# Optimization experiments

Measured on AMD Instinct MI355X. Metric: run time of the kernel, lower is better.

Reference implementation:

```python
import jax, jax.numpy as jnp
import numpy as np
from jax import lax

B, N, C, T = 8, 2000, 32, 12
K, F_CHEV, F_TIME = 3, 64, 64
LN_EPS = 1e-5


def setup_inputs() -> dict:
    key = jax.random.key(0)
    ks = jax.random.split(key, 20)
    s = 0.1
    return {
        "x": jax.random.normal(ks[0], (B, N, C, T), jnp.float32),
        "cheb_polys": jax.random.normal(ks[1], (K, N, N), jnp.float32) * 0.02,
        # temporal attention params
        "U1": jax.random.normal(ks[2], (N,), jnp.float32) * s,
        "U2": jax.random.normal(ks[3], (C, N), jnp.float32) * s,
        "U3": jax.random.normal(ks[4], (C,), jnp.float32) * s,
        "be": jax.random.normal(ks[5], (1, T, T), jnp.float32) * s,
        "Ve": jax.random.normal(ks[6], (T, T), jnp.float32) * s,
        # spatial attention params
        "W1": jax.random.normal(ks[7], (T,), jnp.float32) * s,
        "W2": jax.random.normal(ks[8], (C, T), jnp.float32) * s,
        "W3": jax.random.normal(ks[9], (C,), jnp.float32) * s,
        "bs": jax.random.normal(ks[10], (1, N, N), jnp.float32) * s,
        "Vs": jax.random.normal(ks[11], (N, N), jnp.float32) * (s / np.sqrt(N)),
        # Chebyshev conv params, stacked (K, C, F_chev)
        "Theta": jax.random.normal(ks[12], (K, C, F_CHEV), jnp.float32) * (1.0 / np.sqrt(C)),
        # time conv (1x3) and residual conv (1x1), NCHW/OIHW layout
        "tc_w": jax.random.normal(ks[13], (F_TIME, F_CHEV, 1, 3), jnp.float32) * (1.0 / np.sqrt(3 * F_CHEV)),
        "tc_b": jnp.zeros((F_TIME,), jnp.float32),
        "rc_w": jax.random.normal(ks[14], (F_TIME, C, 1, 1), jnp.float32) * (1.0 / np.sqrt(C)),
        "rc_b": jnp.zeros((F_TIME,), jnp.float32),
        # LayerNorm over nb_time_filter
        "ln_g": jnp.ones((F_TIME,), jnp.float32),
        "ln_b": jnp.zeros((F_TIME,), jnp.float32),
    }


def _conv2d(x, w, b, stride_t):
    # x: (B, Cin, N, T), w: (Cout, Cin, kh, kw)
    pad_w = (w.shape[3] - 1) // 2
    y = lax.conv_general_dilated(
        x, w, window_strides=(1, stride_t),
        padding=[(0, 0), (pad_w, pad_w)],
        dimension_numbers=("NCHW", "OIHW", "NCHW"))
    return y + b[None, :, None, None]


def reference(x, cheb_polys, U1, U2, U3, be, Ve, W1, W2, W3, bs, Vs,
              Theta, tc_w, tc_b, rc_w, rc_b, ln_g, ln_b):
    b, n, c, t = x.shape

    # ---- temporal attention: (B, T, T) ----
    lhs = jnp.einsum("bnct,n->btc", x, U1)              # x.permute(0,3,2,1) @ U1
    lhs = jnp.einsum("btc,cn->btn", lhs, U2)
    rhs = jnp.einsum("c,bnct->bnt", U3, x)
    E = jnp.einsum("ij,bjk->bik", Ve,
                   jax.nn.sigmoid(jnp.einsum("btn,bnu->btu", lhs, rhs) + be))
    temporal_At = jax.nn.softmax(E, axis=1)             # (B, T, T)

    # apply temporal attention
    x_TAt = jnp.matmul(x.reshape(b, n * c, t), temporal_At).reshape(b, n, c, t)

    # ---- spatial attention on x_TAt: (B, N, N) ----
    lhs_s = jnp.einsum("bnct,t->bnc", x_TAt, W1)
    lhs_s = jnp.einsum("bnc,ct->bnt", lhs_s, W2)
    rhs_s = jnp.einsum("c,bnct->btn", W3, x_TAt)        # (W3 @ x).transpose(-1,-2)
    S = jnp.einsum("ij,bjk->bik", Vs,
                   jax.nn.sigmoid(jnp.einsum("bnt,btm->bnm", lhs_s, rhs_s) + bs))
    spatial_At = jax.nn.softmax(S, axis=1)              # (B, N, N)

    # ---- Chebyshev graph conv with spatial attention ----
    # A[b,k,j,i] = cheb[k,j,i] * SAt[b,j,i]; out = relu(sum_k A^T x Theta_k)
    A = cheb_polys[None, :, :, :] * spatial_At[:, None, :, :]   # (B, K, N, N)
    h = jnp.einsum("bkji,bjct->bkitc", A, x)                    # (B, K, N, T, C)
    spatial_gcn = jax.nn.relu(jnp.einsum("bkitc,kcf->bift", h, Theta))  # (B, N, F, T)

    # ---- temporal conv + residual + LayerNorm ----
    time_out = _conv2d(spatial_gcn.transpose(0, 2, 1, 3), tc_w, tc_b, 1)  # (B, F_time, N, T')
    x_res = _conv2d(x.transpose(0, 2, 1, 3), rc_w, rc_b, 1)               # (B, F_time, N, T')
    z = jax.nn.relu(x_res + time_out).transpose(0, 3, 2, 1)               # (B, T', N, F_time)

    mu = jnp.mean(z, axis=-1, keepdims=True)
    var = jnp.mean((z - mu) ** 2, axis=-1, keepdims=True)
    zn = (z - mu) * lax.rsqrt(var + LN_EPS) * ln_g + ln_b

    return zn.transpose(0, 2, 3, 1)                                       # (B, N, F_time, T')
```

## Files before the change

### kernel.cpp

```cpp
#include <hip/hip_runtime.h>
#include <hip/hip_bf16.h>
#include <math.h>

#define B_ 8
#define N_ 2000
#define C_ 32
#define T_ 12
#define K_ 3
#define FC_ 64
#define FT_ 64
#define PW 2048

typedef short bf16x8 __attribute__((ext_vector_type(8)));
typedef float f32x4 __attribute__((ext_vector_type(4)));

__device__ __forceinline__ float sigmoidf(float v) { return 1.0f / (1.0f + __expf(-v)); }
__device__ __forceinline__ float bf2f(unsigned short u) {
    union { unsigned int i; float f; } v; v.i = ((unsigned int)u) << 16; return v.f;
}
__device__ __forceinline__ unsigned short f2bf(float f) {
    union { __hip_bfloat16 h; unsigned short u; } v; v.h = __float2bfloat16(f); return v.u;
}
typedef const __attribute__((address_space(1))) void* gas_t;
typedef __attribute__((address_space(3))) void* las_t;
__device__ __forceinline__ void gload16(const unsigned short* g, unsigned short* l) {
    __builtin_amdgcn_global_load_lds((gas_t)g, (las_t)l, 16, 0, 0);
}

__global__ __launch_bounds__(256) void k_tprep(const float* __restrict__ x, const float* __restrict__ U1,
                                               const float* __restrict__ U3,
                                               float* __restrict__ rhsT, float* __restrict__ plh) {
    int b = blockIdx.y, chunk = blockIdx.x;
    int tid = threadIdx.x;
    int nl = tid >> 5, c = tid & 31;
    int w = tid >> 6;
    float u3 = U3[c];
    float plA[12];
#pragma unroll
    for (int t = 0; t < 12; ++t) plA[t] = 0.f;
    for (int it = 0; it < 5; ++it) {
        int n = chunk * 40 + it * 8 + nl;
        const float* xp = x + ((size_t)(b * 2000 + n) * 32 + c) * 12;
        float4 v0 = *(const float4*)xp, v1 = *(const float4*)(xp + 4), v2 = *(const float4*)(xp + 8);
        float xv[12] = {v0.x, v0.y, v0.z, v0.w, v1.x, v1.y, v1.z, v1.w, v2.x, v2.y, v2.z, v2.w};
        float rv[12];
#pragma unroll
        for (int t = 0; t < 12; ++t) rv[t] = u3 * xv[t];
#pragma unroll
        for (int off = 16; off >= 1; off >>= 1)
#pragma unroll
            for (int t = 0; t < 12; ++t) rv[t] += __shfl_xor(rv[t], off);
        if (c == 0) {
#pragma unroll
            for (int t = 0; t < 12; ++t) rhsT[(size_t)(b * 2000 + n) * 12 + t] = rv[t];
        }
        float u1 = U1[n];
#pragma unroll
        for (int t = 0; t < 12; ++t) plA[t] += u1 * xv[t];
    }
#pragma unroll
    for (int t = 0; t < 12; ++t) plA[t] += __shfl_xor(plA[t], 32);
    __shared__ float accs[4][32][12];
    if ((tid & 63) < 32) {
#pragma unroll
        for (int t = 0; t < 12; ++t) accs[w][c][t] = plA[t];
    }
    __syncthreads();
    if (tid < 384) {
        int c2 = tid / 12, t2 = tid % 12;
        float s = accs[0][c2][t2] + accs[1][c2][t2] + accs[2][c2][t2] + accs[3][c2][t2];
        plh[((size_t)(b * 50 + chunk)) * 384 + tid] = s;
    }
}

__global__ __launch_bounds__(256) void k_tred(const float* __restrict__ plh, float* __restrict__ lhs1) {
    int b = blockIdx.x;
    for (int q = threadIdx.x; q < 384; q += 256) {
        const float* p = plh + (size_t)b * 50 * 384 + q;
        float s = 0.f;
        for (int ch = 0; ch < 50; ++ch) s += p[(size_t)ch * 384];
        int c = q / 12, t = q % 12;
        lhs1[(b * 12 + t) * 32 + c] = s;
    }
}

__global__ __launch_bounds__(256) void k_lhsT(const float* __restrict__ lhs1, const float* __restrict__ U2,
                                              float* __restrict__ lhsT) {
    int gid = blockIdx.x * 256 + threadIdx.x;
    if (gid >= B_ * T_ * N_) return;
    int n = gid % N_;
    int bt = gid / N_;
    const float* l1 = lhs1 + bt * C_;
    float a = 0.f;
#pragma unroll
    for (int c = 0; c < C_; ++c) a += l1[c] * U2[c * N_ + n];
    lhsT[gid] = a;
}

__global__ __launch_bounds__(256) void k_tatt1(const float* __restrict__ lhsT, const float* __restrict__ rhsT,
                                               float* __restrict__ pP) {
    int b = blockIdx.y, ch = blockIdx.x;
    int tid = threadIdx.x;
    int n0 = ch * 125;
    __shared__ float sL[12][128];
    __shared__ float sR[128][12];
    for (int q = tid; q < 12 * 125; q += 256) {
        int t = q / 125, nn = q % 125;
        sL[t][nn] = lhsT[(size_t)(b * 12 + t) * 2000 + n0 + nn];
    }
    for (int q = tid; q < 125 * 12; q += 256) {
        int nn = q / 12, t = q % 12;
        sR[nn][t] = rhsT[(size_t)(b * 2000 + n0 + nn) * 12 + t];
    }
    __syncthreads();
    if (tid < 144) {
        int tP = tid / 12, uP = tid % 12;
        float a = 0.f;
#pragma unroll 5
        for (int nn = 0; nn < 125; ++nn) a += sL[tP][nn] * sR[nn][uP];
        pP[(size_t)(b * 16 + ch) * 144 + tid] = a;
    }
}

__global__ __launch_bounds__(256) void k_tatt2(const float* __restrict__ pP, const float* __restrict__ be,
                                               const float* __restrict__ Ve, float* __restrict__ At) {
    int b = blockIdx.x, tid = threadIdx.x;
    __shared__ float sp[144], sE[144], mk[12], sk[12];
    int tP = tid / 12, uP = tid % 12;
    if (tid < 144) {
        float a = 0.f;
#pragma unroll
        for (int ch = 0; ch < 16; ++ch) a += pP[(size_t)(b * 16 + ch) * 144 + tid];
        sp[tid] = sigmoidf(a + be[tid]);
    }
    __syncthreads();
    if (tid < 144) {
        float e = 0.f;
#pragma unroll
        for (int j = 0; j < 12; ++j) e += Ve[tP * 12 + j] * sp[j * 12 + uP];
        sE[tid] = e;
    }
    __syncthreads();
    if (tid < 12) {
        float m = -1e30f;
#pragma unroll
        for (int i = 0; i < 12; ++i) m = fmaxf(m, sE[i * 12 + tid]);
        float s = 0.f;
#pragma unroll
        for (int i = 0; i < 12; ++i) s += __expf(sE[i * 12 + tid] - m);
        mk[tid] = m; sk[tid] = 1.0f / s;
    }
    __syncthreads();
    if (tid < 144) At[b * 144 + tid] = __expf(sE[tid] - mk[uP]) * sk[uP];
}

__global__ __launch_bounds__(256) void k_xsp(const float* __restrict__ x, const float* __restrict__ At,
                                             const float* __restrict__ W1, const float* __restrict__ W2,
                                             const float* __restrict__ W3,
                                             float* __restrict__ lhs_s, float* __restrict__ rhs_s) {
    int b = blockIdx.y, chunk = blockIdx.x;
    int tid = threadIdx.x, nl = tid >> 5, c = tid & 31;
    int n = chunk * 8 + nl;
    __shared__ float atl[144];
    __shared__ float w2l[384];
    __shared__ float w1l[12];
    if (tid < 144) atl[tid] = At[b * 144 + tid];
    if (tid >= 144 && tid < 156) w1l[tid - 144] = W1[tid - 144];
    for (int q = tid; q < 384; q += 256) w2l[q] = W2[q];
    __syncthreads();
    const float* xp = x + ((size_t)(b * 2000 + n) * 32 + c) * 12;
    float4 v0 = *(const float4*)xp, v1 = *(const float4*)(xp + 4), v2 = *(const float4*)(xp + 8);
    float xv[12] = {v0.x, v0.y, v0.z, v0.w, v1.x, v1.y, v1.z, v1.w, v2.x, v2.y, v2.z, v2.w};
    float xa[12];
#pragma unroll
    for (int t = 0; t < 12; ++t) {
        float s = 0.f;
#pragma unroll
        for (int u = 0; u < 12; ++u) s += xv[u] * atl[u * 12 + t];
        xa[t] = s;
    }
    float w3 = W3[c];
    float rv[12], lv[12];
    float l1 = 0.f;
#pragma unroll
    for (int t = 0; t < 12; ++t) l1 += xa[t] * w1l[t];
#pragma unroll
    for (int t = 0; t < 12; ++t) { rv[t] = w3 * xa[t]; lv[t] = l1 * w2l[c * 12 + t]; }
#pragma unroll
    for (int off = 16; off >= 1; off >>= 1)
#pragma unroll
        for (int t = 0; t < 12; ++t) { rv[t] += __shfl_xor(rv[t], off); lv[t] += __shfl_xor(lv[t], off); }
    if (c == 0) {
#pragma unroll
        for (int t = 0; t < 12; ++t) rhs_s[(size_t)(b * 12 + t) * 2000 + n] = rv[t];
#pragma unroll
        for (int t = 0; t < 12; ++t) lhs_s[(size_t)(b * 2000 + n) * 12 + t] = lv[t];
    }
}

__global__ __launch_bounds__(256) void k_wprep(const float* __restrict__ tc_w, const float* __restrict__ rc_w,
                                               float* __restrict__ tcwT, float* __restrict__ rcwT) {
    int gid = blockIdx.x * 256 + threadIdx.x;
    if (gid < 12288) {
        int fi = gid / 192, rem = gid % 192, f = rem / 3, d = rem % 3;
        tcwT[gid] = tc_w[(f * 64 + fi) * 3 + d];
    } else if (gid < 14336) {
        int q = gid - 12288;
        int c = q >> 6, f = q & 63;
        rcwT[q] = rc_w[f * 32 + c];
    }
}

__global__ __launch_bounds__(256) void k_vsb(const float* __restrict__ Vs, unsigned short* __restrict__ Vsb) {
    int gid = blockIdx.x * 256 + threadIdx.x;
    int row = gid >> 8, chunk = gid & 255;
    int p0 = chunk * 8;
    unsigned short o[8];
#pragma unroll
    for (int e = 0; e < 8; ++e) {
        int p = p0 + e;
        o[e] = (row < N_ && p < N_) ? f2bf(Vs[row * N_ + p]) : (unsigned short)0;
    }
    *(int4*)(Vsb + (size_t)row * PW + p0) = *(int4*)o;
}

__global__ __launch_bounds__(256) void k_chebT(const float* __restrict__ cheb, unsigned short* __restrict__ chebT) {
    int j0 = blockIdx.x * 64, i0 = blockIdx.y * 64, kk = blockIdx.z;
    __shared__ float Tl[64][65];
    int t = threadIdx.x;
    int rr = t >> 2, c0 = (t & 3) * 16;
    int j = j0 + rr;
#pragma unroll
    for (int e = 0; e < 16; ++e) {
        int i = i0 + c0 + e;
        Tl[rr][c0 + e] = (j < N_ && i < N_) ? cheb[(size_t)kk * 4000000 + (size_t)j * N_ + i] : 0.f;
    }
    __syncthreads();
    int l = t & 63, w = t >> 6;
    unsigned short o[16];
#pragma unroll
    for (int e = 0; e < 16; ++e) o[e] = f2bf(Tl[w * 16 + e][l]);
    unsigned short* dst = chebT + (size_t)kk * PW * PW + (size_t)(i0 + l) * PW + j0 + w * 16;
    *(int4*)dst = *(int4*)o;
    *(int4*)(dst + 8) = *(int4*)(o + 8);
}

__global__ __launch_bounds__(256) void k_xT(const float* __restrict__ x, unsigned short* __restrict__ xT) {
    int j0 = blockIdx.x * 64, r0 = blockIdx.y * 64, b = blockIdx.z;
    __shared__ float Tl[64][65];
    int t = threadIdx.x;
    int rr = t >> 2, c0 = (t & 3) * 16;
    int j = j0 + rr;
#pragma unroll
    for (int e = 0; e < 16; ++e) {
        int r = r0 + c0 + e;
        Tl[rr][c0 + e] = (j < N_) ? x[(size_t)(b * N_ + j) * 384 + r] : 0.f;
    }
    __syncthreads();
    int l = t & 63, w = t >> 6;
    unsigned short o[16];
#pragma unroll
    for (int e = 0; e < 16; ++e) o[e] = f2bf(Tl[w * 16 + e][l]);
    unsigned short* dst = xT + (size_t)b * 384 * PW + (size_t)(r0 + l) * PW + j0 + w * 16;
    *(int4*)dst = *(int4*)o;
    *(int4*)(dst + 8) = *(int4*)(o + 8);
}

__global__ __launch_bounds__(256) void k_sig(const float* __restrict__ lhs_s, const float* __restrict__ rhs_s,
                                             const float* __restrict__ bs, unsigned short* __restrict__ sigT) {
    int p0 = blockIdx.x * 64, i0 = blockIdx.y * 64, b = blockIdx.z;
    __shared__ float sL[64][12];
    __shared__ float sR[12][64];
    __shared__ float bsl[64][65];
    int t = threadIdx.x;
    for (int q = t; q < 768; q += 256) {
        int pp = q / 12, tt = q % 12;
        int p = p0 + pp;
        sL[pp][tt] = (p < N_) ? lhs_s[(b * N_ + p) * 12 + tt] : 0.f;
    }
    for (int q = t; q < 768; q += 256) {
        int tt = q >> 6, ii = q & 63;
        int i = i0 + ii;
        sR[tt][ii] = (i < N_) ? rhs_s[b * (T_ * N_) + tt * N_ + i] : 0.f;
    }
    {
        int pp = t >> 2, c0 = (t & 3) * 16;
        int p = p0 + pp;
        if (p < N_ && i0 + c0 + 15 < N_) {
            const float* src = bs + (size_t)p * N_ + i0 + c0;
#pragma unroll
            for (int e = 0; e < 16; e += 4) *(float4*)&bsl[pp][c0 + e] = *(const float4*)(src + e);
        } else {
#pragma unroll
            for (int e = 0; e < 16; ++e) {
                int i = i0 + c0 + e;
                bsl[pp][c0 + e] = (p < N_ && i < N_) ? bs[(size_t)p * N_ + i] : 0.f;
            }
        }
    }
    __syncthreads();
    int ii = t & 63, w = t >> 6;
    int i = i0 + ii;
    unsigned short o[16];
#pragma unroll
    for (int e = 0; e < 16; ++e) {
        int pl = w * 16 + e;
        int p = p0 + pl;
        float v = 0.f;
        if (p < N_ && i < N_) {
            float d = bsl[pl][ii];
#pragma unroll
            for (int tt = 0; tt < 12; ++tt) d += sL[pl][tt] * sR[tt][ii];
            v = sigmoidf(d);
        }
        o[e] = f2bf(v);
    }
    unsigned short* dst = sigT + (size_t)b * PW * PW + (size_t)i * PW + p0 + w * 16;
    *(int4*)dst = *(int4*)o;
    *(int4*)(dst + 8) = *(int4*)(o + 8);
}

__global__ __launch_bounds__(256) void k_gemm_S_mfma(const unsigned short* __restrict__ Vsb,
                                                     const unsigned short* __restrict__ sigT,
                                                     unsigned short* __restrict__ ST) {
    int b = blockIdx.z;
    int j0 = blockIdx.x * 128, i0 = blockIdx.y * 128;
    const unsigned short* Ap = sigT + (size_t)b * PW * PW;
    __shared__ unsigned short As[2][4096];
    __shared__ unsigned short Bs[2][4096];
    int t = threadIdx.x, lane = t & 63, w = t >> 6;
    int wr = w >> 1, wc = w & 1;
    f32x4 acc[4][4];
#pragma unroll
    for (int a = 0; a < 4; ++a)
#pragma unroll
        for (int c = 0; c < 4; ++c)
#pragma unroll
            for (int q = 0; q < 4; ++q) acc[a][c][q] = 0.f;
    int srow = t >> 2;
    int sseg = (t & 3) ^ (srow & 3);
    const unsigned short* gA = Ap + (size_t)(i0 + srow) * PW + sseg * 8;
    const unsigned short* gB = Vsb + (size_t)(j0 + srow) * PW + sseg * 8;
    int ldso = w * 512;
#define STAGE_S(buf, p) do { \
    gload16(gA + (p), &As[buf][ldso]); \
    gload16(gA + 64 * PW + (p), &As[buf][2048 + ldso]); \
    gload16(gB + (p), &Bs[buf][ldso]); \
    gload16(gB + 64 * PW + (p), &Bs[buf][2048 + ldso]); \
} while (0)
    STAGE_S(0, 0);
    __syncthreads();
    int cur = 0;
    int rswz = ((lane >> 4) ^ (lane & 3)) * 8;
    for (int p = 0; p < PW; p += 32) {
        if (p + 32 < PW) STAGE_S(cur ^ 1, p + 32);
        bf16x8 af[4], bfr[4];
#pragma unroll
        for (int f = 0; f < 4; ++f) {
            af[f] = *(const bf16x8*)&As[cur][(wr * 64 + f * 16 + (lane & 15)) * 32 + rswz];
            bfr[f] = *(const bf16x8*)&Bs[cur][(wc * 64 + f * 16 + (lane & 15)) * 32 + rswz];
        }
#pragma unroll
        for (int fm = 0; fm < 4; ++fm)
#pragma unroll
            for (int fn = 0; fn < 4; ++fn)
                acc[fm][fn] = __builtin_amdgcn_mfma_f32_16x16x32_bf16(af[fm], bfr[fn], acc[fm][fn], 0, 0, 0);
        __syncthreads();
        cur ^= 1;
    }
#undef STAGE_S
    unsigned short* Sp = ST + (size_t)b * PW * PW;
#pragma unroll
    for (int fm = 0; fm < 4; ++fm) {
        int row0 = i0 + wr * 64 + fm * 16 + ((lane >> 4) << 2);
#pragma unroll
        for (int fn = 0; fn < 4; ++fn) {
            int col = j0 + wc * 64 + fn * 16 + (lane & 15);
#pragma unroll
            for (int q = 0; q < 4; ++q)
                Sp[(size_t)(row0 + q) * PW + col] = f2bf(acc[fm][fn][q]);
        }
    }
}

__global__ __launch_bounds__(256) void k_smrow(const unsigned short* __restrict__ ST,
                                               float* __restrict__ gm, float* __restrict__ gs) {
    int wid = threadIdx.x >> 6, lane = threadIdx.x & 63;
    int b = blockIdx.y;
    int i = blockIdx.x * 4 + wid;
    const unsigned short* rp = ST + (size_t)b * PW * PW + (size_t)i * PW;
    float vals[32];
    float m = -1e30f;
#pragma unroll
    for (int k = 0; k < 4; ++k) {
        int j0 = lane * 8 + k * 512;
        if (j0 < N_) {
            union { int4 v; unsigned short s[8]; } u;
            u.v = *(const int4*)(rp + j0);
#pragma unroll
            for (int e = 0; e < 8; ++e) {
                vals[k * 8 + e] = bf2f(u.s[e]);
                m = fmaxf(m, vals[k * 8 + e]);
            }
        } else {
#pragma unroll
            for (int e = 0; e < 8; ++e) vals[k * 8 + e] = -1e30f;
        }
    }
#pragma unroll
    for (int off = 32; off >= 1; off >>= 1) m = fmaxf(m, __shfl_xor(m, off));
    float s = 0.f;
#pragma unroll
    for (int k = 0; k < 32; ++k) s += __expf(vals[k] - m);
#pragma unroll
    for (int off = 32; off >= 1; off >>= 1) s += __shfl_xor(s, off);
    if (lane == 0) {
        gm[b * 2048 + i] = m;
        gs[b * 2048 + i] = 1.0f / s;
    }
}

__global__ __launch_bounds__(512) void k_gemm_cheb_mfma(const unsigned short* __restrict__ chebT,
                                                        const unsigned short* __restrict__ ST,
                                                        const float* __restrict__ gm, const float* __restrict__ gs,
                                                        const unsigned short* __restrict__ xT,
                                                        unsigned short* __restrict__ h2) {
    int bk = blockIdx.y;
    int b = bk / 3, kk = bk % 3;
    int i0 = blockIdx.x * 128;
    const unsigned short* Ac = chebT + (size_t)kk * PW * PW;
    const unsigned short* Sa = ST + (size_t)b * PW * PW;
    const unsigned short* Bx = xT + (size_t)b * 384 * PW;
    __shared__ unsigned short As[2][4096];
    __shared__ unsigned short Bs[2][12288];
    int t = threadIdx.x, lane = t & 63, w = t >> 6;
    int wr = w >> 2, wc = w & 3;
    f32x4 acc[4][6];
#pragma unroll
    for (int a = 0; a < 4; ++a)
#pragma unroll
        for (int c = 0; c < 6; ++c)
#pragma unroll
            for (int q = 0; q < 4; ++q) acc[a][c][q] = 0.f;
    int arow = t >> 2, aq = t & 3;
    const unsigned short* gc = Ac + (size_t)(i0 + arow) * PW + aq * 8;
    const unsigned short* gsat = Sa + (size_t)(i0 + arow) * PW + aq * 8;
    float gmv = gm[b * 2048 + i0 + arow];
    float gsv = gs[b * 2048 + i0 + arow];
    int aoff = arow * 32 + (aq ^ (arow & 3)) * 8;
    int bseg = (t & 3) ^ ((t >> 2) & 3);
    const unsigned short* gB = Bx + (size_t)(t >> 2) * PW + bseg * 8;
    int ldso = w * 512;
#define STAGE_B(buf, p) do { \
    gload16(gB + (p), &Bs[buf][ldso]); \
    gload16(gB + 128 * PW + (p), &Bs[buf][4096 + ldso]); \
    gload16(gB + 256 * PW + (p), &Bs[buf][8192 + ldso]); \
} while (0)
    union U8 { int4 v; unsigned short s[8]; };
    U8 ca, sa;
    ca.v = *(const int4*)gc;
    sa.v = *(const int4*)gsat;
    STAGE_B(0, 0);
    {
        U8 o;
#pragma unroll
        for (int e = 0; e < 8; ++e) o.s[e] = f2bf(bf2f(ca.s[e]) * __expf(bf2f(sa.s[e]) - gmv) * gsv);
        *(int4*)&As[0][aoff] = o.v;
    }
    ca.v = *(const int4*)(gc + 32);
    sa.v = *(const int4*)(gsat + 32);
    __syncthreads();
    int cur = 0;
    int rswz = ((lane >> 4) ^ (lane & 3)) * 8;
    for (int p = 0; p < PW; p += 32) {
        if (p + 32 < PW) {
            STAGE_B(cur ^ 1, p + 32);
            U8 o;
#pragma unroll
            for (int e = 0; e < 8; ++e) o.s[e] = f2bf(bf2f(ca.s[e]) * __expf(bf2f(sa.s[e]) - gmv) * gsv);
            *(int4*)&As[cur ^ 1][aoff] = o.v;
            int pn = (p + 64 < PW) ? p + 64 : 0;
            ca.v = *(const int4*)(gc + pn);
            sa.v = *(const int4*)(gsat + pn);
        }
        bf16x8 af[4], bfr[6];
#pragma unroll
        for (int fm = 0; fm < 4; ++fm)
            af[fm] = *(const bf16x8*)&As[cur][(wr * 64 + fm * 16 + (lane & 15)) * 32 + rswz];
#pragma unroll
        for (int fn = 0; fn < 6; ++fn)
            bfr[fn] = *(const bf16x8*)&Bs[cur][(wc * 96 + fn * 16 + (lane & 15)) * 32 + rswz];
#pragma unroll
        for (int fm = 0; fm < 4; ++fm)
#pragma unroll
            for (int fn = 0; fn < 6; ++fn)
                acc[fm][fn] = __builtin_amdgcn_mfma_f32_16x16x32_bf16(af[fm], bfr[fn], acc[fm][fn], 0, 0, 0);
        __syncthreads();
        cur ^= 1;
    }
#undef STAGE_B
    unsigned short* hp = h2 + (size_t)bk * 768000;
#pragma unroll
    for (int fm = 0; fm < 4; ++fm) {
        int row0 = i0 + wr * 64 + fm * 16 + ((lane >> 4) << 2);
#pragma unroll
        for (int fn = 0; fn < 6; ++fn) {
            int col = wc * 96 + fn * 16 + (lane & 15);
#pragma unroll
            for (int q = 0; q < 4; ++q) {
                int row = row0 + q;
                if (row < N_) hp[(size_t)row * 384 + col] = f2bf(acc[fm][fn][q]);
            }
        }
    }
}

__global__ __launch_bounds__(512) void k_final3(const float* __restrict__ x, const unsigned short* __restrict__ h2,
                                                const float* __restrict__ ThetaG,
                                                const float* __restrict__ tcwT, const float* __restrict__ tc_b,
                                                const float* __restrict__ rcwT, const float* __restrict__ rc_b,
                                                const float* __restrict__ ln_g, const float* __restrict__ ln_b,
                                                float* __restrict__ out) {
    __shared__ __align__(16) char smem[110848];
    unsigned int* gl = (unsigned int*)smem;
    unsigned short* th = (unsigned short*)(smem + 98560);
    float* red_s = (float*)(smem + 98560);
    float* red_q = red_s + 64 * 13;

    int tid = threadIdx.x;
    int n_l = tid & 63, fg = tid >> 6;
    int b = blockIdx.y;
    int node = blockIdx.x * 64 + n_l;
    bool ok = node < N_;
    int nd = ok ? node : N_ - 1;

    for (int q = tid; q < 6144; q += 512) th[q] = f2bf(ThetaG[q]);
    __syncthreads();

    float acc[8][12];
#pragma unroll
    for (int ff = 0; ff < 8; ++ff)
#pragma unroll
        for (int t = 0; t < 12; ++t) acc[ff][t] = 0.f;
    const unsigned short* hb = h2 + (size_t)b * 3 * 768000 + (size_t)nd * 384;
#pragma unroll
    for (int kk = 0; kk < 3; ++kk) {
        const unsigned short* hp = hb + (size_t)kk * 768000;
#pragma unroll 2
        for (int c = 0; c < 32; ++c) {
            const unsigned short* hq = hp + c * 12;
            uint2 u0 = *(const uint2*)(hq);
            uint2 u1 = *(const uint2*)(hq + 4);
            uint2 u2 = *(const uint2*)(hq + 8);
            float h[12];
            h[0] = bf2f((unsigned short)u0.x);  h[1] = bf2f((unsigned short)(u0.x >> 16));
            h[2] = bf2f((unsigned short)u0.y);  h[3] = bf2f((unsigned short)(u0.y >> 16));
            h[4] = bf2f((unsigned short)u1.x);  h[5] = bf2f((unsigned short)(u1.x >> 16));
            h[6] = bf2f((unsigned short)u1.y);  h[7] = bf2f((unsigned short)(u1.y >> 16));
            h[8] = bf2f((unsigned short)u2.x);  h[9] = bf2f((unsigned short)(u2.x >> 16));
            h[10] = bf2f((unsigned short)u2.y); h[11] = bf2f((unsigned short)(u2.y >> 16));
            const unsigned short* wv = th + (kk * 32 + c) * 64 + fg * 8;
            uint2 w01 = *(const uint2*)wv;
            uint2 w23 = *(const uint2*)(wv + 4);
            float wf[8];
            wf[0] = bf2f((unsigned short)w01.x); wf[1] = bf2f((unsigned short)(w01.x >> 16));
            wf[2] = bf2f((unsigned short)w01.y); wf[3] = bf2f((unsigned short)(w01.y >> 16));
            wf[4] = bf2f((unsigned short)w23.x); wf[5] = bf2f((unsigned short)(w23.x >> 16));
            wf[6] = bf2f((unsigned short)w23.y); wf[7] = bf2f((unsigned short)(w23.y >> 16));
#pragma unroll
            for (int ff = 0; ff < 8; ++ff)
#pragma unroll
                for (int t = 0; t < 12; ++t) acc[ff][t] = fmaf(h[t], wf[ff], acc[ff][t]);
        }
    }
    unsigned int* gr = gl + n_l * 385 + fg * 48;
#pragma unroll
    for (int ff = 0; ff < 8; ++ff)
#pragma unroll
        for (int tp = 0; tp < 6; ++tp) {
            float a0 = fmaxf(acc[ff][2 * tp], 0.f), a1 = fmaxf(acc[ff][2 * tp + 1], 0.f);
            gr[ff * 6 + tp] = (unsigned int)f2bf(a0) | ((unsigned int)f2bf(a1) << 16);
        }
    __syncthreads();

    float z[8][12];
#pragma unroll
    for (int ff = 0; ff < 8; ++ff) {
        float bias = tc_b[fg * 8 + ff] + rc_b[fg * 8 + ff];
#pragma unroll
        for (int t = 0; t < 12; ++t) z[ff][t] = bias;
    }
    const float* xp = x + (size_t)(b * 2000 + nd) * 384;
#pragma unroll 2
    for (int c = 0; c < 32; ++c) {
        float4 x0 = *(const float4*)(xp + c * 12);
        float4 x1 = *(const float4*)(xp + c * 12 + 4);
        float4 x2 = *(const float4*)(xp + c * 12 + 8);
        float xv[12] = {x0.x, x0.y, x0.z, x0.w, x1.x, x1.y, x1.z, x1.w, x2.x, x2.y, x2.z, x2.w};
        float4 r0 = *(const float4*)(rcwT + c * 64 + fg * 8);
        float4 r1 = *(const float4*)(rcwT + c * 64 + fg * 8 + 4);
        float rw[8] = {r0.x, r0.y, r0.z, r0.w, r1.x, r1.y, r1.z, r1.w};
#pragma unroll
        for (int ff = 0; ff < 8; ++ff)
#pragma unroll
            for (int t = 0; t < 12; ++t) z[ff][t] = fmaf(xv[t], rw[ff], z[ff][t]);
    }
    const unsigned int* grow = gl + n_l * 385;
    for (int fi = 0; fi < 64; ++fi) {
        float g[12];
#pragma unroll
        for (int j = 0; j < 6; ++j) {
            unsigned int u = grow[fi * 6 + j];
            g[2 * j] = bf2f((unsigned short)u);
            g[2 * j + 1] = bf2f((unsigned short)(u >> 16));
        }
        const float* wp = tcwT + (fi * 64 + fg * 8) * 3;
        float4 w0 = *(const float4*)(wp);
        float4 w1 = *(const float4*)(wp + 4);
        float4 w2 = *(const float4*)(wp + 8);
        float4 w3 = *(const float4*)(wp + 12);
        float4 w4 = *(const float4*)(wp + 16);
        float4 w5 = *(const float4*)(wp + 20);
        float wb[24] = {w0.x, w0.y, w0.z, w0.w, w1.x, w1.y, w1.z, w1.w,
                        w2.x, w2.y, w2.z, w2.w, w3.x, w3.y, w3.z, w3.w,
                        w4.x, w4.y, w4.z, w4.w, w5.x, w5.y, w5.z, w5.w};
#pragma unroll
        for (int ff = 0; ff < 8; ++ff) {
            float a0 = wb[ff * 3], a1 = wb[ff * 3 + 1], a2 = wb[ff * 3 + 2];
            z[ff][0] = fmaf(g[0], a1, fmaf(g[1], a2, z[ff][0]));
#pragma unroll
            for (int t = 1; t < 11; ++t)
                z[ff][t] = fmaf(g[t - 1], a0, fmaf(g[t], a1, fmaf(g[t + 1], a2, z[ff][t])));
            z[ff][11] = fmaf(g[10], a0, fmaf(g[11], a1, z[ff][11]));
        }
    }
#pragma unroll
    for (int ff = 0; ff < 8; ++ff)
#pragma unroll
        for (int t = 0; t < 12; ++t) z[ff][t] = fmaxf(z[ff][t], 0.f);

    float s[12], q[12];
#pragma unroll
    for (int t = 0; t < 12; ++t) { s[t] = 0.f; q[t] = 0.f; }
#pragma unroll
    for (int ff = 0; ff < 8; ++ff)
#pragma unroll
        for (int t = 0; t < 12; ++t) { s[t] += z[ff][t]; q[t] += z[ff][t] * z[ff][t]; }
    __syncthreads();
    for (int g = 0; g < 8; ++g) {
        if (fg == g) {
            if (g == 0) {
#pragma unroll
                for (int t = 0; t < 12; ++t) { red_s[n_l * 13 + t] = s[t]; red_q[n_l * 13 + t] = q[t]; }
            } else {
#pragma unroll
                for (int t = 0; t < 12; ++t) { red_s[n_l * 13 + t] += s[t]; red_q[n_l * 13 + t] += q[t]; }
            }
        }
        __syncthreads();
    }
    float mu[12], rs[12];
#pragma unroll
    for (int t = 0; t < 12; ++t) {
        float m = red_s[n_l * 13 + t] * (1.0f / 64.0f);
        float v = red_q[n_l * 13 + t] * (1.0f / 64.0f) - m * m;
        mu[t] = m;
        rs[t] = rsqrtf(v + 1e-5f);
    }
    if (ok) {
        float* op = out + ((size_t)(b * 2000 + node) * 64 + fg * 8) * 12;
#pragma unroll
        for (int ff = 0; ff < 8; ++ff) {
            float lg = ln_g[fg * 8 + ff], lb = ln_b[fg * 8 + ff];
            float o[12];
#pragma unroll
            for (int t = 0; t < 12; ++t) o[t] = (z[ff][t] - mu[t]) * rs[t] * lg + lb;
#pragma unroll
            for (int tq = 0; tq < 3; ++tq)
                *(float4*)(op + ff * 12 + tq * 4) = make_float4(o[tq * 4], o[tq * 4 + 1], o[tq * 4 + 2], o[tq * 4 + 3]);
        }
    }
}

extern "C" void kernel_launch(void* const* d_in, const int* in_sizes, int n_in,
                              void* d_out, int out_size, void* d_ws, size_t ws_size,
                              hipStream_t stream) {
    const float* x     = (const float*)d_in[0];
    const float* cheb  = (const float*)d_in[1];
    const float* U1    = (const float*)d_in[2];
    const float* U2    = (const float*)d_in[3];
    const float* U3    = (const float*)d_in[4];
    const float* be    = (const float*)d_in[5];
    const float* Ve    = (const float*)d_in[6];
    const float* W1    = (const float*)d_in[7];
    const float* W2    = (const float*)d_in[8];
    const float* W3    = (const float*)d_in[9];
    const float* bs    = (const float*)d_in[10];
    const float* Vs    = (const float*)d_in[11];
    const float* Theta = (const float*)d_in[12];
    const float* tc_w  = (const float*)d_in[13];
    const float* tc_b  = (const float*)d_in[14];
    const float* rc_w  = (const float*)d_in[15];
    const float* rc_b  = (const float*)d_in[16];
    const float* ln_g  = (const float*)d_in[17];
    const float* ln_b  = (const float*)d_in[18];
    float* out = (float*)d_out;

    float* ws    = (float*)d_ws;
    float* At    = ws;
    float* lhs1  = ws + 1152;
    float* lhsT  = ws + 4224;
    float* rhsT  = ws + 196224;
    float* lhs_s = ws + 388224;
    float* rhs_s = ws + 580224;
    float* gm    = ws + 772224;
    float* gs    = ws + 788608;
    float* tcwT  = ws + 804992;
    float* rcwT  = ws + 817280;
    float* plh   = ws + 819328;
    float* pP    = ws + 972928;
    unsigned short* Vsb   = (unsigned short*)(ws + 991360);
    unsigned short* chebT = (unsigned short*)(ws + 3088512);
    unsigned short* xT    = (unsigned short*)(ws + 9379968);
    unsigned short* sigT  = (unsigned short*)(ws + 12525696);
    unsigned short* h2    = sigT;
    unsigned short* STb   = (unsigned short*)(ws + 29302912);

    k_wprep<<<56, 256, 0, stream>>>(tc_w, rc_w, tcwT, rcwT);
    k_vsb<<<2048, 256, 0, stream>>>(Vs, Vsb);
    k_chebT<<<dim3(32, 32, 3), 256, 0, stream>>>(cheb, chebT);
    k_xT<<<dim3(32, 6, 8), 256, 0, stream>>>(x, xT);
    k_tprep<<<dim3(50, 8), 256, 0, stream>>>(x, U1, U3, rhsT, plh);
    k_tred<<<8, 256, 0, stream>>>(plh, lhs1);
    k_lhsT<<<750, 256, 0, stream>>>(lhs1, U2, lhsT);
    k_tatt1<<<dim3(16, 8), 256, 0, stream>>>(lhsT, rhsT, pP);
    k_tatt2<<<8, 256, 0, stream>>>(pP, be, Ve, At);
    k_xsp<<<dim3(250, 8), 256, 0, stream>>>(x, At, W1, W2, W3, lhs_s, rhs_s);
    k_sig<<<dim3(32, 32, 8), 256, 0, stream>>>(lhs_s, rhs_s, bs, sigT);
    k_gemm_S_mfma<<<dim3(16, 16, 8), 256, 0, stream>>>(Vsb, sigT, STb);
    k_smrow<<<dim3(512, 8), 256, 0, stream>>>(STb, gm, gs);
    k_gemm_cheb_mfma<<<dim3(16, 24), 512, 0, stream>>>(chebT, STb, gm, gs, xT, h2);
    k_final3<<<dim3(32, 8), 512, 0, stream>>>(x, h2, Theta, tcwT, tc_b, rcwT, rc_b, ln_g, ln_b, out);
}
```

Baseline: 646.2 us.

## Triple-buffer S GEMM loads and swizzle block order for L2 locality

The Vs x sigmoid GEMM moves from a double-buffered LDS pipeline with two full barriers per step to a three-stage ring. Explicit vmcnt waits allow one tile's global-to-LDS loads to stay in flight while the current tile is computed, with a single barrier per iteration. The block index is also remapped so consecutively scheduled blocks come from different batches/tiles, presumably to spread memory traffic across L2/channels. Costs are 50% more LDS, which may lower occupancy, and correctness depends on the hand-counted vmcnt value.

```diff
diff --git a/kernel.cpp b/kernel.cpp
--- a/kernel.cpp
+++ b/kernel.cpp
@@ -323,11 +323,14 @@
 __global__ __launch_bounds__(256) void k_gemm_S_mfma(const unsigned short* __restrict__ Vsb,
                                                      const unsigned short* __restrict__ sigT,
                                                      unsigned short* __restrict__ ST) {
-    int b = blockIdx.z;
-    int j0 = blockIdx.x * 128, i0 = blockIdx.y * 128;
+    int lid = blockIdx.x + (blockIdx.y << 4) + (blockIdx.z << 8);
+    int swz = (lid & 7) * 256 + (lid >> 3);
+    int j0 = (swz & 15) * 128;
+    int i0 = ((swz >> 4) & 15) * 128;
+    int b = swz >> 8;
     const unsigned short* Ap = sigT + (size_t)b * PW * PW;
-    __shared__ unsigned short As[2][4096];
-    __shared__ unsigned short Bs[2][4096];
+    __shared__ unsigned short As[3][4096];
+    __shared__ unsigned short Bs[3][4096];
     int t = threadIdx.x, lane = t & 63, w = t >> 6;
     int wr = w >> 1, wc = w & 1;
     f32x4 acc[4][4];
@@ -349,24 +352,31 @@
     gload16(gB + 64 * PW + (p), &Bs[buf][2048 + ldso]); \
 } while (0)
     STAGE_S(0, 0);
-    __syncthreads();
-    int cur = 0;
+    STAGE_S(1, 32);
+    int s0 = 0, s1 = 1, s2 = 2;
     int rswz = ((lane >> 4) ^ (lane & 3)) * 8;
-    for (int p = 0; p < PW; p += 32) {
-        if (p + 32 < PW) STAGE_S(cur ^ 1, p + 32);
+    const int nk = PW / 32;
+    for (int k = 0; k < nk; ++k) {
+        if (k < nk - 1) {
+            asm volatile("s_waitcnt vmcnt(4)" ::: "memory");
+        } else {
+            asm volatile("s_waitcnt vmcnt(0)" ::: "memory");
+        }
+        __builtin_amdgcn_sched_barrier(0);
+        __builtin_amdgcn_s_barrier();
+        if (k + 2 < nk) STAGE_S(s2, (k + 2) * 32);
         bf16x8 af[4], bfr[4];
 #pragma unroll
         for (int f = 0; f < 4; ++f) {
-            af[f] = *(const bf16x8*)&As[cur][(wr * 64 + f * 16 + (lane & 15)) * 32 + rswz];
-            bfr[f] = *(const bf16x8*)&Bs[cur][(wc * 64 + f * 16 + (lane & 15)) * 32 + rswz];
+            af[f] = *(const bf16x8*)&As[s0][(wr * 64 + f * 16 + (lane & 15)) * 32 + rswz];
+            bfr[f] = *(const bf16x8*)&Bs[s0][(wc * 64 + f * 16 + (lane & 15)) * 32 + rswz];
         }
 #pragma unroll
         for (int fm = 0; fm < 4; ++fm)
 #pragma unroll
             for (int fn = 0; fn < 4; ++fn)
                 acc[fm][fn] = __builtin_amdgcn_mfma_f32_16x16x32_bf16(af[fm], bfr[fn], acc[fm][fn], 0, 0, 0);
-        __syncthreads();
-        cur ^= 1;
+        int tmp = s0; s0 = s1; s1 = s2; s2 = tmp;
     }
 #undef STAGE_S
     unsigned short* Sp = ST + (size_t)b * PW * PW;
```

Result: no change. 643.1 us (-0.5%).

## Enlarge S GEMM tiles to 256x256 with 4-stage async pipeline and block swizzle

Applied to the files above, without the earlier changes.

Rewrites the batched Vs×sigmoid GEMM kernel to use 256x256 output tiles with 512 threads and 8x4 MFMA fragments per wave, raising arithmetic intensity per LDS load. Replaces the double-buffered loop with a 4-slot prefetch ring using explicit vmcnt waits and a single barrier per k-step. Also adds a block-index swizzle and raises MFMA issue priority. The cost is more LDS (128KB) and more accumulator registers, which lowers occupancy, and the grid shrinks to 512 blocks.

```diff
diff --git a/kernel.cpp b/kernel.cpp
--- a/kernel.cpp
+++ b/kernel.cpp
@@ -320,65 +320,74 @@
     *(int4*)(dst + 8) = *(int4*)(o + 8);
 }
 
-__global__ __launch_bounds__(256) void k_gemm_S_mfma(const unsigned short* __restrict__ Vsb,
+__global__ __launch_bounds__(512) void k_gemm_S_mfma(const unsigned short* __restrict__ Vsb,
                                                      const unsigned short* __restrict__ sigT,
                                                      unsigned short* __restrict__ ST) {
-    int b = blockIdx.z;
-    int j0 = blockIdx.x * 128, i0 = blockIdx.y * 128;
+    int lid = blockIdx.x + (blockIdx.y << 3) + (blockIdx.z << 6);
+    int swz = (lid & 7) * 64 + (lid >> 3);
+    int j0 = (swz & 7) * 256;
+    int i0 = ((swz >> 3) & 7) * 256;
+    int b = swz >> 6;
     const unsigned short* Ap = sigT + (size_t)b * PW * PW;
-    __shared__ unsigned short As[2][4096];
-    __shared__ unsigned short Bs[2][4096];
+    __shared__ unsigned short As[4][8192];
+    __shared__ unsigned short Bs[4][8192];
     int t = threadIdx.x, lane = t & 63, w = t >> 6;
-    int wr = w >> 1, wc = w & 1;
-    f32x4 acc[4][4];
-#pragma unroll
-    for (int a = 0; a < 4; ++a)
-#pragma unroll
-        for (int c = 0; c < 4; ++c)
-#pragma unroll
-            for (int q = 0; q < 4; ++q) acc[a][c][q] = 0.f;
+    int wr = w >> 2, wc = w & 3;
+    f32x4 acc[8][4];
+#pragma unroll
+    for (int m = 0; m < 8; ++m)
+#pragma unroll
+        for (int n = 0; n < 4; ++n)
+#pragma unroll
+            for (int q = 0; q < 4; ++q) acc[m][n][q] = 0.f;
     int srow = t >> 2;
     int sseg = (t & 3) ^ (srow & 3);
     const unsigned short* gA = Ap + (size_t)(i0 + srow) * PW + sseg * 8;
     const unsigned short* gB = Vsb + (size_t)(j0 + srow) * PW + sseg * 8;
-    int ldso = w * 512;
-#define STAGE_S(buf, p) do { \
-    gload16(gA + (p), &As[buf][ldso]); \
-    gload16(gA + 64 * PW + (p), &As[buf][2048 + ldso]); \
-    gload16(gB + (p), &Bs[buf][ldso]); \
-    gload16(gB + 64 * PW + (p), &Bs[buf][2048 + ldso]); \
+    int ldw = w * 512;
+#define STG(slot, kt) do { \
+    gload16(gA + (size_t)(kt) * 32, &As[slot][ldw]); \
+    gload16(gA + (size_t)128 * PW + (size_t)(kt) * 32, &As[slot][4096 + ldw]); \
+    gload16(gB + (size_t)(kt) * 32, &Bs[slot][ldw]); \
+    gload16(gB + (size_t)128 * PW + (size_t)(kt) * 32, &Bs[slot][4096 + ldw]); \
 } while (0)
-    STAGE_S(0, 0);
-    __syncthreads();
-    int cur = 0;
-    int rswz = ((lane >> 4) ^ (lane & 3)) * 8;
-    for (int p = 0; p < PW; p += 32) {
-        if (p + 32 < PW) STAGE_S(cur ^ 1, p + 32);
-        bf16x8 af[4], bfr[4];
-#pragma unroll
-        for (int f = 0; f < 4; ++f) {
-            af[f] = *(const bf16x8*)&As[cur][(wr * 64 + f * 16 + (lane & 15)) * 32 + rswz];
-            bfr[f] = *(const bf16x8*)&Bs[cur][(wc * 64 + f * 16 + (lane & 15)) * 32 + rswz];
-        }
-#pragma unroll
-        for (int fm = 0; fm < 4; ++fm)
-#pragma unroll
-            for (int fn = 0; fn < 4; ++fn)
-                acc[fm][fn] = __builtin_amdgcn_mfma_f32_16x16x32_bf16(af[fm], bfr[fn], acc[fm][fn], 0, 0, 0);
-        __syncthreads();
-        cur ^= 1;
-    }
-#undef STAGE_S
+    STG(0, 0); STG(1, 1); STG(2, 2);
+    int l15 = lane & 15;
+    int swr = ((lane >> 4) ^ (lane & 3)) * 8;
+    int abase = (wr * 128 + l15) * 32 + swr;
+    int bbase = (wc * 64 + l15) * 32 + swr;
+    for (int kt = 0; kt < 64; ++kt) {
+        if (kt < 62)       asm volatile("s_waitcnt vmcnt(8)" ::: "memory");
+        else if (kt == 62) asm volatile("s_waitcnt vmcnt(4)" ::: "memory");
+        else               asm volatile("s_waitcnt vmcnt(0)" ::: "memory");
+        __builtin_amdgcn_s_barrier();
+        __builtin_amdgcn_sched_barrier(0);
+        if (kt + 3 < 64) STG((kt + 3) & 3, kt + 3);
+        int slot = kt & 3;
+        bf16x8 af[8], bfv[4];
+#pragma unroll
+        for (int m = 0; m < 8; ++m) af[m] = *(const bf16x8*)&As[slot][abase + m * 512];
+#pragma unroll
+        for (int n = 0; n < 4; ++n) bfv[n] = *(const bf16x8*)&Bs[slot][bbase + n * 512];
+        __builtin_amdgcn_s_setprio(1);
+#pragma unroll
+        for (int m = 0; m < 8; ++m)
+#pragma unroll
+            for (int n = 0; n < 4; ++n)
+                acc[m][n] = __builtin_amdgcn_mfma_f32_16x16x32_bf16(af[m], bfv[n], acc[m][n], 0, 0, 0);
+        __builtin_amdgcn_s_setprio(0);
+    }
+#undef STG
     unsigned short* Sp = ST + (size_t)b * PW * PW;
 #pragma unroll
-    for (int fm = 0; fm < 4; ++fm) {
-        int row0 = i0 + wr * 64 + fm * 16 + ((lane >> 4) << 2);
-#pragma unroll
-        for (int fn = 0; fn < 4; ++fn) {
-            int col = j0 + wc * 64 + fn * 16 + (lane & 15);
+    for (int m = 0; m < 8; ++m) {
+        int row0 = i0 + wr * 128 + m * 16 + ((lane >> 4) << 2);
+#pragma unroll
+        for (int n = 0; n < 4; ++n) {
+            int col = j0 + wc * 64 + n * 16 + (lane & 15);
 #pragma unroll
             for (int q = 0; q < 4; ++q)
-                Sp[(size_t)(row0 + q) * PW + col] = f2bf(acc[fm][fn][q]);
+                Sp[(size_t)(row0 + q) * PW + col] = f2bf(acc[m][n][q]);
         }
     }
 }
@@ -737,7 +746,7 @@
     k_tatt2<<<8, 256, 0, stream>>>(pP, be, Ve, At);
     k_xsp<<<dim3(250, 8), 256, 0, stream>>>(x, At, W1, W2, W3, lhs_s, rhs_s);
     k_sig<<<dim3(32, 32, 8), 256, 0, stream>>>(lhs_s, rhs_s, bs, sigT);
-    k_gemm_S_mfma<<<dim3(16, 16, 8), 256, 0, stream>>>(Vsb, sigT, STb);
+    k_gemm_S_mfma<<<dim3(8, 8, 8), 512, 0, stream>>>(Vsb, sigT, STb);
     k_smrow<<<dim3(512, 8), 256, 0, stream>>>(STb, gm, gs);
     k_gemm_cheb_mfma<<<dim3(16, 24), 512, 0, stream>>>(chebT, STb, gm, gs, xT, h2);
     k_final3<<<dim3(32, 8), 512, 0, stream>>>(x, h2, Theta, tcwT, tc_b, rcwT, rc_b, ln_g, ln_b, out);
```

After: 645.4 us. Within noise of the previous version (-0.1%).
